# Performance work log

Hardware: AMD Instinct MI355X
Metric: run time of the kernel (lower is better)

## Reference

```python
import jax, jax.numpy as jnp
import numpy as np

B, S, D = 2, 2048, 1024
NH, NKV = 16, 4
HD = D // NH
KVD = NKV * HD
NE, MM = 8, 4
INTER = MM * D // NE  # 512
ROPE_BASE = 10000.0
ALPHA, BETA, GATE, DT = 0.95, 0.3, 0.1, 0.1
MU_MIN, MU_MAX, VMAX = 0.5, 1.5, 3.0


def rms_norm(x):
    # torch F.rms_norm with eps=None -> finfo(dtype).eps, no learned weight
    return x * jax.lax.rsqrt(jnp.mean(x * x, axis=-1, keepdims=True) + jnp.finfo(x.dtype).eps)


def rope_tables(seq_len, dtype):
    inv_freq = 1.0 / ROPE_BASE ** (jnp.arange(0, HD, 2, dtype=jnp.float32) / HD)
    t = jnp.arange(seq_len, dtype=jnp.float32)
    freqs = jnp.outer(t, inv_freq)  # [S, HD/2]
    return jnp.cos(freqs).astype(dtype)[None, None], jnp.sin(freqs).astype(dtype)[None, None]


def apply_rotary(x, cos, sin):
    half = x.shape[-1] // 2
    x1, x2 = x[..., :half], x[..., half:]
    return jnp.concatenate((x1 * cos + x2 * sin, -x1 * sin + x2 * cos), axis=-1)


def attention(n, cq_w, ck_w, cv_w, proj_w, q_gain):
    q = jnp.einsum('bsd,od->bso', n, cq_w).reshape(B, S, NH, HD).transpose(0, 2, 1, 3)
    k = jnp.einsum('bsd,od->bso', n, ck_w).reshape(B, S, NKV, HD).transpose(0, 2, 1, 3)
    v = jnp.einsum('bsd,od->bso', n, cv_w).reshape(B, S, NKV, HD).transpose(0, 2, 1, 3)
    q, k = rms_norm(q), rms_norm(k)
    cos, sin = rope_tables(S, q.dtype)
    q, k = apply_rotary(q, cos, sin), apply_rotary(k, cos, sin)
    q = q * q_gain[None, :, None, None]
    rep = NH // NKV  # GQA: repeat kv heads
    k = jnp.repeat(k, rep, axis=1)
    v = jnp.repeat(v, rep, axis=1)
    scale = 1.0 / np.sqrt(HD).astype(np.float32)
    scores = jnp.einsum('bhqd,bhkd->bhqk', q, k) * scale
    causal = jnp.tril(jnp.ones((S, S), bool))
    scores = jnp.where(causal[None, None], scores, jnp.finfo(scores.dtype).min)
    probs = jax.nn.softmax(scores, axis=-1)
    y = jnp.einsum('bhqk,bhkd->bhqd', probs, v)
    y = y.transpose(0, 2, 1, 3).reshape(B, S, D)
    return jnp.einsum('bsd,od->bso', y, proj_w)


def moe(m, gate_up, down, eids):
    # faithful to TokenRoutedMLP: dense per-expert GEMM, masked accumulate
    flat = m.reshape(-1, D)
    fids = eids.reshape(-1)
    out = jnp.zeros_like(flat)
    for e in range(NE):
        gu = flat @ gate_up[e]                       # [T, 2*INTER]
        g, u = gu[:, :INTER], gu[:, INTER:]
        h = (jax.nn.silu(g) * u) @ down[e]           # [T, D]
        out = out + h * (fids == e)[:, None].astype(flat.dtype)
    return out.reshape(B, S, D)


def setup_inputs():
    key = jax.random.key(0)
    ks = jax.random.split(key, 10)
    w = lambda k, shape: jax.random.normal(k, shape, jnp.float32) * 0.02
    return {
        'x': jax.random.normal(ks[0], (B, S, D), jnp.float32),
        'x0': jax.random.normal(ks[1], (B, S, D), jnp.float32),
        'vel': jnp.zeros((B, S, D), jnp.float32),
        'resid_mix': jnp.stack((jnp.ones(D, jnp.float32), jnp.zeros(D, jnp.float32))),
        'attn_scale': jnp.ones(D, jnp.float32),
        'mlp_scale': jnp.ones(D, jnp.float32),
        'cq_w': w(ks[2], (D, D)),
        'ck_w': w(ks[3], (KVD, D)),
        'cv_w': w(ks[4], (KVD, D)),
        'proj_w': w(ks[5], (D, D)),
        'q_gain': jnp.ones(NH, jnp.float32),
        'mu': jnp.full((D,), 1.0, jnp.float32),
        'gate_up': w(ks[6], (NE, D, 2 * INTER)),
        'down': w(ks[7], (NE, INTER, D)),
        'eids': jax.random.randint(ks[8], (B, S), 0, NE),
    }


def reference(x, x0, vel, resid_mix, attn_scale, mlp_scale, cq_w, ck_w, cv_w, proj_w, q_gain, mu, gate_up, down, eids):
    x = resid_mix[0][None, None, :] * x + resid_mix[1][None, None, :] * x0
    n = rms_norm(x)
    x = x + attn_scale[None, None, :] * attention(n, cq_w, ck_w, cv_w, proj_w, q_gain)
    # PID dynamics
    mu_c = jnp.clip(mu, MU_MIN, MU_MAX)
    v_next = jnp.clip(ALPHA * vel - BETA * (x - mu_c[None, None, :]), -VMAX, VMAX)
    x = x + DT * GATE * v_next
    x = x + mlp_scale[None, None, :] * moe(rms_norm(x), gate_up, down, eids)
    return x, v_next
```

## Files before the change

kernel.cpp:

```cpp
#include <hip/hip_runtime.h>
#include <hip/hip_bf16.h>
#include <math.h>

#define NBATCH 2
#define NSEQ   2048
#define NDIM   1024
#define NHEAD  16
#define NKVH   4
#define HDIM   64
#define KVD    256
#define NEXP   8
#define NINTER 512
#define NTOK   (NBATCH*NSEQ)
#define QKVN   1536
#define MAXTILE 40
#define RMS_EPS 1.1920929e-07f
#define LN_10000 9.210340371976184f
#define QSCALE (0.125f * 1.44269504088896f)
#define DEFER_THR 11.5f

typedef __attribute__((ext_vector_type(8))) short bf16x8;
typedef __attribute__((ext_vector_type(4))) short short4v;
typedef __attribute__((ext_vector_type(4))) float f32x4;

__device__ __forceinline__ short f2b(float f) {
  return __builtin_bit_cast(short, (__bf16)f);
}
__device__ __forceinline__ float b2f(short s) {
  unsigned u = ((unsigned)(unsigned short)s) << 16;
  return __builtin_bit_cast(float, u);
}
__device__ __forceinline__ float ex2(float x) {
  float r; asm("v_exp_f32 %0, %1" : "=v"(r) : "v"(x)); return r;
}
__device__ __forceinline__ void load_lds16(const short* g, short* l) {
  __builtin_amdgcn_global_load_lds((const __attribute__((address_space(1))) void*)g,
                                   (__attribute__((address_space(3))) void*)l, 16, 0, 0);
}

__device__ __forceinline__ float wred64(float v) {
#pragma unroll
  for (int m = 32; m >= 1; m >>= 1) v += __shfl_xor(v, m);
  return v;
}

__global__ __launch_bounds__(256) void k_w_prep(
    const float* __restrict__ cq, const float* __restrict__ ck,
    const float* __restrict__ cv, const float* __restrict__ pw,
    const float* __restrict__ gate_up,
    short* __restrict__ wqkv, short* __restrict__ wproj, short* __restrict__ wgu_t) {
  __shared__ short T[64*66];
  const int bid = blockIdx.x;
  const int t = threadIdx.x;
  if (bid < 2560) {
    const int row = bid;
    const int c = t * 4;
    const float* src; short* dst;
    if (row < 1024)      { src = cq + (size_t)row*NDIM;        dst = wqkv + (size_t)row*NDIM; }
    else if (row < 1280) { src = ck + (size_t)(row-1024)*NDIM; dst = wqkv + (size_t)row*NDIM; }
    else if (row < 1536) { src = cv + (size_t)(row-1280)*NDIM; dst = wqkv + (size_t)row*NDIM; }
    else                 { src = pw + (size_t)(row-1536)*NDIM; dst = wproj + (size_t)(row-1536)*NDIM; }
    float4 v = *(const float4*)(src + c);
    short4v o = {f2b(v.x), f2b(v.y), f2b(v.z), f2b(v.w)};
    *(short4v*)(dst + c) = o;
  } else {
    const int b2 = bid - 2560;
    const int kt = b2 & 15, nt = (b2 >> 4) & 15, e = b2 >> 8;
    const float* ie = gate_up + (size_t)e*1024*1024 + (size_t)(kt*64)*1024 + nt*64;
    short* oe = wgu_t + (size_t)e*1024*1024 + (size_t)(nt*64)*1024 + kt*64;
    const int r = t >> 4, c = (t & 15) * 4;
#pragma unroll
    for (int p = 0; p < 4; ++p) {
      float4 v = *(const float4*)(ie + (size_t)(p*16 + r)*1024 + c);
      T[(p*16 + r)*66 + c + 0] = f2b(v.x);
      T[(p*16 + r)*66 + c + 1] = f2b(v.y);
      T[(p*16 + r)*66 + c + 2] = f2b(v.z);
      T[(p*16 + r)*66 + c + 3] = f2b(v.w);
    }
    __syncthreads();
#pragma unroll
    for (int p = 0; p < 4; ++p) {
      int rr = p*16 + r;
      short4v o = {T[(c+0)*66 + rr], T[(c+1)*66 + rr], T[(c+2)*66 + rr], T[(c+3)*66 + rr]};
      *(short4v*)(oe + (size_t)rr*1024 + c) = o;
    }
  }
}

__global__ __launch_bounds__(256) void k_w_transpose(
    const float* __restrict__ in, short* __restrict__ outp, int KIN, int NIN) {
  __shared__ short T[64*66];
  const int kt = blockIdx.x, nt = blockIdx.y, e = blockIdx.z;
  const float* ie = in + (size_t)e*KIN*NIN + (size_t)(kt*64)*NIN + nt*64;
  short* oe = outp + (size_t)e*NIN*KIN + (size_t)(nt*64)*KIN + kt*64;
  const int t = threadIdx.x;
  const int r = t >> 4, c = (t & 15) * 4;
#pragma unroll
  for (int p = 0; p < 4; ++p) {
    float4 v = *(const float4*)(ie + (size_t)(p*16 + r)*NIN + c);
    T[(p*16 + r)*66 + c + 0] = f2b(v.x);
    T[(p*16 + r)*66 + c + 1] = f2b(v.y);
    T[(p*16 + r)*66 + c + 2] = f2b(v.z);
    T[(p*16 + r)*66 + c + 3] = f2b(v.w);
  }
  __syncthreads();
#pragma unroll
  for (int p = 0; p < 4; ++p) {
    int rr = p*16 + r;
    short4v o = {T[(c+0)*66 + rr], T[(c+1)*66 + rr], T[(c+2)*66 + rr], T[(c+3)*66 + rr]};
    *(short4v*)(oe + (size_t)rr*KIN + c) = o;
  }
}

__global__ __launch_bounds__(256) void k_resid_rms(
    const float* __restrict__ x, const float* __restrict__ x0,
    const float* __restrict__ rmix, short* __restrict__ xr, short* __restrict__ nrm) {
  const int row = blockIdx.x;
  const int t = threadIdx.x;
  const int d = t * 4;
  const size_t base = (size_t)row * NDIM + d;
  float4 a  = *(const float4*)(x  + base);
  float4 b  = *(const float4*)(x0 + base);
  float4 m0 = *(const float4*)(rmix + d);
  float4 m1 = *(const float4*)(rmix + NDIM + d);
  float4 r;
  r.x = m0.x*a.x + m1.x*b.x;
  r.y = m0.y*a.y + m1.y*b.y;
  r.z = m0.z*a.z + m1.z*b.z;
  r.w = m0.w*a.w + m1.w*b.w;
  float ss = r.x*r.x + r.y*r.y + r.z*r.z + r.w*r.w;
  ss = wred64(ss);
  __shared__ float wsum[4];
  if ((t & 63) == 0) wsum[t >> 6] = ss;
  __syncthreads();
  float tot = wsum[0] + wsum[1] + wsum[2] + wsum[3];
  float rms = rsqrtf(tot * (1.0f/NDIM) + RMS_EPS);
  short4v xo = {f2b(r.x), f2b(r.y), f2b(r.z), f2b(r.w)};
  short4v no = {f2b(r.x*rms), f2b(r.y*rms), f2b(r.z*rms), f2b(r.w*rms)};
  *(short4v*)(xr + base) = xo;
  *(short4v*)(nrm + base) = no;
}

template <int MODE>
__global__ __launch_bounds__(256) void k_gemm_mfma(
    const short* __restrict__ A, int lda,
    const short* __restrict__ Bw, int K, int N,
    short* __restrict__ Cb, float* __restrict__ Cf, int ldc,
    const int* __restrict__ rowmap, const int* __restrict__ tiletab,
    const int* __restrict__ meta, const float* __restrict__ mscale) {
  __shared__ short sA[128*32];
  __shared__ short sB[128*32];
  int row0, end = 0x7fffffff, e = 0;
  if (MODE == 0) {
    row0 = blockIdx.y * 128;
  } else {
    e = tiletab[2*blockIdx.y];
    if (e < 0) return;
    row0 = tiletab[2*blockIdx.y + 1];
    end = meta[1 + e];
  }
  const int t = threadIdx.x;
  const int w = t >> 6, l = t & 63;
  const int wr = (w >> 1) * 64, wc = (w & 1) * 64;
  const int lrow = l & 15, lk8 = (l >> 4) * 8;
  const int srow0 = w*16 + (l >> 2);
  const int scol = (l & 3) * 8;
  const short* Bp = Bw + (size_t)e * N * K + (size_t)(blockIdx.x * 128) * K;
  const short* gA0;
  const short* gA1;
  if (MODE == 1) {
    int s0 = row0 + srow0;      if (s0 >= NTOK) s0 = NTOK - 1;
    int s1 = row0 + 64 + srow0; if (s1 >= NTOK) s1 = NTOK - 1;
    gA0 = A + (size_t)rowmap[s0] * lda + scol;
    gA1 = A + (size_t)rowmap[s1] * lda + scol;
  } else {
    gA0 = A + (size_t)(row0 + srow0) * lda + scol;
    gA1 = A + (size_t)(row0 + 64 + srow0) * lda + scol;
  }
  const short* gB0 = Bp + (size_t)srow0 * K + scol;
  const short* gB1 = Bp + (size_t)(64 + srow0) * K + scol;
  short* lA0 = sA + (w*16)*32;
  short* lA1 = sA + (64 + w*16)*32;
  short* lB0 = sB + (w*16)*32;
  short* lB1 = sB + (64 + w*16)*32;
  f32x4 acc[4][4];
#pragma unroll
  for (int m = 0; m < 4; ++m)
#pragma unroll
    for (int n = 0; n < 4; ++n) acc[m][n] = 0.f;
  for (int k0 = 0; k0 < K; k0 += 32) {
    __syncthreads();
    load_lds16(gA0, lA0);
    load_lds16(gA1, lA1);
    load_lds16(gB0, lB0);
    load_lds16(gB1, lB1);
    gA0 += 32; gA1 += 32; gB0 += 32; gB1 += 32;
    __syncthreads();
    bf16x8 af[4], bfr[4];
#pragma unroll
    for (int m = 0; m < 4; ++m)
      af[m] = *(const bf16x8*)&sA[(wr + m*16 + lrow)*32 + lk8];
#pragma unroll
    for (int n = 0; n < 4; ++n)
      bfr[n] = *(const bf16x8*)&sB[(wc + n*16 + lrow)*32 + lk8];
#pragma unroll
    for (int m = 0; m < 4; ++m)
#pragma unroll
      for (int n = 0; n < 4; ++n)
        acc[m][n] = __builtin_amdgcn_mfma_f32_16x16x32_bf16(af[m], bfr[n], acc[m][n], 0, 0, 0);
  }
  const int col0 = blockIdx.x * 128;
  if (MODE <= 1) {
#pragma unroll
    for (int m = 0; m < 4; ++m) {
#pragma unroll
      for (int r = 0; r < 4; ++r) {
        int rr = row0 + wr + m*16 + (l >> 4)*4 + r;
        if (rr < end) {
#pragma unroll
          for (int n = 0; n < 4; ++n)
            Cb[(size_t)rr * ldc + col0 + wc + n*16 + lrow] = f2b(acc[m][n][r]);
        }
      }
    }
  } else {
#pragma unroll
    for (int m = 0; m < 4; ++m) {
#pragma unroll
      for (int r = 0; r < 4; ++r) {
        int slot = row0 + wr + m*16 + (l >> 4)*4 + r;
        if (slot < end) {
          int tok = rowmap[slot];
#pragma unroll
          for (int n = 0; n < 4; ++n) {
            int cc = col0 + wc + n*16 + lrow;
            Cf[(size_t)tok * ldc + cc] += mscale[cc] * acc[m][n][r];
          }
        }
      }
    }
  }
}

__global__ __launch_bounds__(256) void k_qk_norm_rope(
    short* __restrict__ qkv, const float* __restrict__ q_gain) {
  const int row = blockIdx.x;
  const int t = threadIdx.x;
  const int w = t >> 6, lane = t & 63;
  const int s = row & (NSEQ - 1);
  const int fi = lane & 31;
  const float fr = (float)s * expf(-(float)fi * (LN_10000 / 32.0f));
  const float co = cosf(fr), si = sinf(fr);
#pragma unroll
  for (int h = w; h < NHEAD; h += 4) {
    short* p = qkv + (size_t)row*QKVN + h*HDIM + lane;
    float v = b2f(*p);
    float ssum = wred64(v*v);
    float rr = rsqrtf(ssum * (1.0f/HDIM) + RMS_EPS);
    float vn = v * rr;
    float partner = __shfl_xor(vn, 32);
    float o = (lane < 32) ? (vn*co + partner*si) : (vn*co - partner*si);
    *p = f2b(o * q_gain[h] * QSCALE);
  }
  if (w < NKVH) {
    short* p = qkv + (size_t)row*QKVN + 1024 + w*HDIM + lane;
    float v = b2f(*p);
    float ssum = wred64(v*v);
    float rr = rsqrtf(ssum * (1.0f/HDIM) + RMS_EPS);
    float vn = v * rr;
    float partner = __shfl_xor(vn, 32);
    float o = (lane < 32) ? (vn*co + partner*si) : (vn*co - partner*si);
    *p = f2b(o);
  }
}

__global__ __launch_bounds__(256) void k_transpose_v(
    const short* __restrict__ qkv, short* __restrict__ vbT) {
  __shared__ short T[64*72];
  const int blk = blockIdx.x;
  const int st = blk & 31, kh = (blk >> 5) & 3, b = blk >> 7;
  const int t = threadIdx.x;
#pragma unroll
  for (int i = 0; i < 2; ++i) {
    int c = t + i*256;
    int s = c >> 3, d0 = (c & 7) * 8;
    bf16x8 v = *(const bf16x8*)(qkv + (size_t)(b*NSEQ + st*64 + s)*QKVN + 1280 + kh*HDIM + d0);
#pragma unroll
    for (int j = 0; j < 8; ++j) T[(d0 + j)*72 + s] = v[j];
  }
  __syncthreads();
#pragma unroll
  for (int i = 0; i < 2; ++i) {
    int c = t + i*256;
    int d = c >> 3, s0 = (c & 7) * 8;
    *(bf16x8*)(vbT + (size_t)((b*NKVH + kh)*HDIM + d)*NSEQ + st*64 + s0) = *(bf16x8*)&T[d*72 + s0];
  }
}

__global__ __launch_bounds__(256) void k_attn_mfma(
    const short* __restrict__ qkv, const short* __restrict__ vbT, short* __restrict__ y) {
  __shared__ short Ks[2][64*72];
  __shared__ short Vt[2][64*72];
  __shared__ short Ps[64*72];
  const int t = threadIdx.x;
  const int l = t & 63, w = t >> 6;
  const int lrow = l & 15, g = l >> 4, lk8 = g * 8;
  const int bid = blockIdx.x;
  int qt = bid & 15;
  const int h = (bid >> 4) & 15, b = bid >> 8;
  if (b & 1) qt = 15 - qt;
  const int kh = h >> 2;
  bf16x8 qf[2][2];
#pragma unroll
  for (int qra = 0; qra < 2; ++qra) {
    int qrow_g = b*NSEQ + qt*128 + qra*64 + w*16 + lrow;
#pragma unroll
    for (int hf = 0; hf < 2; ++hf)
      qf[qra][hf] = *(const bf16x8*)(qkv + (size_t)qrow_g*QKVN + h*HDIM + hf*32 + lk8);
  }
  const int r0a = t >> 3;
  const int d0a = (t & 7) * 8;
  const short* kgbase = qkv + 1024 + (size_t)kh*HDIM;
  const short* vgbase = vbT + (size_t)((b*NKVH + kh)*HDIM)*NSEQ;
  bf16x8 kr0, kr1, vr0, vr1;
#define LOADKV(KT) do { \
    kr0 = *(const bf16x8*)(kgbase + (size_t)(b*NSEQ + (KT)*64 + r0a)*QKVN + d0a); \
    kr1 = *(const bf16x8*)(kgbase + (size_t)(b*NSEQ + (KT)*64 + r0a + 32)*QKVN + d0a); \
    vr0 = *(const bf16x8*)(vgbase + (size_t)r0a*NSEQ + (KT)*64 + d0a); \
    vr1 = *(const bf16x8*)(vgbase + (size_t)(r0a + 32)*NSEQ + (KT)*64 + d0a); \
  } while (0)
  float m_i[2] = {-INFINITY, -INFINITY};
  float l_i[2] = {0.f, 0.f};
  f32x4 O[2][4];
#pragma unroll
  for (int qra = 0; qra < 2; ++qra)
#pragma unroll
    for (int db = 0; db < 4; ++db) O[qra][db] = 0.f;
  const int ktmax = 2*qt + 1;
  LOADKV(0);
  for (int kt = 0; kt <= ktmax; ++kt) {
    const int buf = kt & 1;
    *(bf16x8*)&Ks[buf][r0a*72 + d0a] = kr0;
    *(bf16x8*)&Ks[buf][(r0a + 32)*72 + d0a] = kr1;
    *(bf16x8*)&Vt[buf][r0a*72 + d0a] = vr0;
    *(bf16x8*)&Vt[buf][(r0a + 32)*72 + d0a] = vr1;
    __syncthreads();
    if (kt < ktmax) LOADKV(kt + 1);
    bf16x8 kf[4][2];
#pragma unroll
    for (int nb = 0; nb < 4; ++nb) {
      kf[nb][0] = *(const bf16x8*)&Ks[buf][(nb*16 + lrow)*72 + lk8];
      kf[nb][1] = *(const bf16x8*)&Ks[buf][(nb*16 + lrow)*72 + 32 + lk8];
    }
    const int qra0 = (kt == ktmax) ? 1 : 0;
    bf16x8 pf[2][2];
#pragma unroll
    for (int qra = 0; qra < 2; ++qra) {
      if (qra >= qra0) {
        f32x4 sc[4];
#pragma unroll
        for (int nb = 0; nb < 4; ++nb) sc[nb] = 0.f;
        __builtin_amdgcn_s_setprio(1);
#pragma unroll
        for (int nb = 0; nb < 4; ++nb) {
          sc[nb] = __builtin_amdgcn_mfma_f32_16x16x32_bf16(kf[nb][0], qf[qra][0], sc[nb], 0, 0, 0);
          sc[nb] = __builtin_amdgcn_mfma_f32_16x16x32_bf16(kf[nb][1], qf[qra][1], sc[nb], 0, 0, 0);
        }
        __builtin_amdgcn_s_setprio(0);
        if (kt >= 2*qt) {
          int qg = qt*128 + qra*64 + w*16 + lrow;
#pragma unroll
          for (int nb = 0; nb < 4; ++nb)
#pragma unroll
            for (int r = 0; r < 4; ++r)
              if (kt*64 + nb*16 + g*4 + r > qg) sc[nb][r] = -INFINITY;
        }
        float rm = sc[0][0];
#pragma unroll
        for (int nb = 0; nb < 4; ++nb)
#pragma unroll
          for (int r = 0; r < 4; ++r) rm = fmaxf(rm, sc[nb][r]);
        rm = fmaxf(rm, __shfl_xor(rm, 16));
        rm = fmaxf(rm, __shfl_xor(rm, 32));
        if (!__all(rm <= m_i[qra] + DEFER_THR)) {
          float mn = fmaxf(m_i[qra], rm);
          float fac = ex2(m_i[qra] - mn);
          l_i[qra] *= fac;
          m_i[qra] = mn;
#pragma unroll
          for (int r = 0; r < 4; ++r) {
            float ff = __shfl(fac, g*4 + r);
#pragma unroll
            for (int db = 0; db < 4; ++db) O[qra][db][r] *= ff;
          }
        }
        float rs = 0.f;
#pragma unroll
        for (int nb = 0; nb < 4; ++nb) {
#pragma unroll
          for (int r = 0; r < 4; ++r) {
            float p = ex2(sc[nb][r] - m_i[qra]);
            sc[nb][r] = p;
            rs += p;
          }
        }
        rs += __shfl_xor(rs, 16);
        rs += __shfl_xor(rs, 32);
        l_i[qra] += rs;
        short* prow = &Ps[(w*16 + lrow)*72];
#pragma unroll
        for (int nb = 0; nb < 4; ++nb) {
          short4v pk = {f2b(sc[nb][0]), f2b(sc[nb][1]), f2b(sc[nb][2]), f2b(sc[nb][3])};
          *(short4v*)(prow + nb*16 + g*4) = pk;
        }
        pf[qra][0] = *(const bf16x8*)&Ps[(w*16 + lrow)*72 + lk8];
        pf[qra][1] = *(const bf16x8*)&Ps[(w*16 + lrow)*72 + 32 + lk8];
      }
    }
    __builtin_amdgcn_s_setprio(1);
#pragma unroll
    for (int db = 0; db < 4; ++db) {
      bf16x8 vf0 = *(const bf16x8*)&Vt[buf][(db*16 + lrow)*72 + lk8];
      bf16x8 vf1 = *(const bf16x8*)&Vt[buf][(db*16 + lrow)*72 + 32 + lk8];
      if (qra0 == 0) {
        O[0][db] = __builtin_amdgcn_mfma_f32_16x16x32_bf16(pf[0][0], vf0, O[0][db], 0, 0, 0);
        O[0][db] = __builtin_amdgcn_mfma_f32_16x16x32_bf16(pf[0][1], vf1, O[0][db], 0, 0, 0);
      }
      O[1][db] = __builtin_amdgcn_mfma_f32_16x16x32_bf16(pf[1][0], vf0, O[1][db], 0, 0, 0);
      O[1][db] = __builtin_amdgcn_mfma_f32_16x16x32_bf16(pf[1][1], vf1, O[1][db], 0, 0, 0);
    }
    __builtin_amdgcn_s_setprio(0);
  }
#undef LOADKV
#pragma unroll
  for (int qra = 0; qra < 2; ++qra) {
    float linv = 1.0f / l_i[qra];
#pragma unroll
    for (int r = 0; r < 4; ++r) {
      float inv = __shfl(linv, g*4 + r);
      int rowo = b*NSEQ + qt*128 + qra*64 + w*16 + g*4 + r;
#pragma unroll
      for (int db = 0; db < 4; ++db)
        y[(size_t)rowo*NDIM + h*HDIM + db*16 + lrow] = f2b(O[qra][db][r] * inv);
    }
  }
}

__global__ __launch_bounds__(256) void k_fuse_vel(
    const short* __restrict__ xr, const short* __restrict__ aout,
    const float* __restrict__ vel, const float* __restrict__ ascale,
    const float* __restrict__ mu, float* __restrict__ out, short* __restrict__ mbuf) {
  const int row = blockIdx.x;
  const int t = threadIdx.x;
  const int d = t * 4;
  const size_t base = (size_t)row * NDIM + d;
  short4v a4 = *(const short4v*)(xr + base);
  short4v o4 = *(const short4v*)(aout + base);
  float4 vv = *(const float4*)(vel + base);
  float4 as = *(const float4*)(ascale + d);
  float4 mu4 = *(const float4*)(mu + d);
  float xs[4], vns[4];
  const float asl[4] = {as.x, as.y, as.z, as.w};
  const float mul[4] = {mu4.x, mu4.y, mu4.z, mu4.w};
  const float vvl[4] = {vv.x, vv.y, vv.z, vv.w};
#pragma unroll
  for (int i = 0; i < 4; ++i) {
    float x1 = b2f(a4[i]) + asl[i] * b2f(o4[i]);
    float muc = fminf(fmaxf(mul[i], 0.5f), 1.5f);
    float vn = fminf(fmaxf(0.95f*vvl[i] - 0.3f*(x1 - muc), -3.f), 3.f);
    xs[i] = x1 + 0.01f*vn;
    vns[i] = vn;
  }
  float4 x2 = {xs[0], xs[1], xs[2], xs[3]};
  float4 vnq = {vns[0], vns[1], vns[2], vns[3]};
  *(float4*)(out + base) = x2;
  *(float4*)(out + (size_t)NTOK*NDIM + base) = vnq;
  float ss = xs[0]*xs[0] + xs[1]*xs[1] + xs[2]*xs[2] + xs[3]*xs[3];
  ss = wred64(ss);
  __shared__ float wsum[4];
  if ((t & 63) == 0) wsum[t >> 6] = ss;
  __syncthreads();
  float tot = wsum[0] + wsum[1] + wsum[2] + wsum[3];
  float rms = rsqrtf(tot * (1.0f/NDIM) + RMS_EPS);
  short4v m4 = {f2b(xs[0]*rms), f2b(xs[1]*rms), f2b(xs[2]*rms), f2b(xs[3]*rms)};
  *(short4v*)(mbuf + base) = m4;
}

__global__ __launch_bounds__(256) void k_route(
    const int* __restrict__ eids, int* __restrict__ rowmap,
    int* __restrict__ tiletab, int* __restrict__ meta) {
  __shared__ int cnt[NEXP];
  __shared__ int ctr[NEXP];
  const int t = threadIdx.x;
  if (t < NEXP) cnt[t] = 0;
  __syncthreads();
  for (int i = t; i < NTOK; i += 256) atomicAdd(&cnt[eids[i]], 1);
  __syncthreads();
  if (t == 0) {
    int off = 0, tile = 0;
    for (int e = 0; e < NEXP; ++e) {
      ctr[e] = off;
      int nt_e = (cnt[e] + 127) >> 7;
      for (int j = 0; j < nt_e; ++j) { tiletab[2*tile] = e; tiletab[2*tile+1] = off + j*128; ++tile; }
      off += cnt[e];
      meta[1 + e] = off;
    }
    meta[0] = tile;
    for (int j = tile; j < MAXTILE; ++j) { tiletab[2*j] = -1; tiletab[2*j+1] = 0; }
  }
  __syncthreads();
  for (int i = t; i < NTOK; i += 256) {
    int e = eids[i];
    int slot = atomicAdd(&ctr[e], 1);
    rowmap[slot] = i;
  }
}

__global__ __launch_bounds__(256) void k_silu(
    const short* __restrict__ gu, short* __restrict__ hb) {
  int gid = blockIdx.x * 256 + threadIdx.x;
  int row = gid >> 7, c4 = (gid & 127) * 4;
  short4v g = *(const short4v*)(gu + (size_t)row*1024 + c4);
  short4v u = *(const short4v*)(gu + (size_t)row*1024 + 512 + c4);
  short4v o;
#pragma unroll
  for (int i = 0; i < 4; ++i) {
    float gf = b2f(g[i]), uf = b2f(u[i]);
    o[i] = f2b(gf / (1.0f + __expf(-gf)) * uf);
  }
  *(short4v*)(hb + (size_t)row*512 + c4) = o;
}

extern "C" void kernel_launch(void* const* d_in, const int* in_sizes, int n_in,
                              void* d_out, int out_size, void* d_ws, size_t ws_size,
                              hipStream_t stream) {
  const float* x      = (const float*)d_in[0];
  const float* x0     = (const float*)d_in[1];
  const float* vel    = (const float*)d_in[2];
  const float* rmix   = (const float*)d_in[3];
  const float* ascale = (const float*)d_in[4];
  const float* mscale = (const float*)d_in[5];
  const float* cq_w   = (const float*)d_in[6];
  const float* ck_w   = (const float*)d_in[7];
  const float* cv_w   = (const float*)d_in[8];
  const float* proj_w = (const float*)d_in[9];
  const float* q_gain = (const float*)d_in[10];
  const float* mu     = (const float*)d_in[11];
  const float* gate_up= (const float*)d_in[12];
  const float* down   = (const float*)d_in[13];
  const int*   eids   = (const int*)d_in[14];
  float* out = (float*)d_out;
  char* base = (char*)d_ws;

  const size_t MB = 1024*1024;
  short* wqkv  = (short*)base;
  short* wproj = (short*)(base + 3*MB);
  int*   rowmap  = (int*)(base + 5*MB);
  int*   tiletab = rowmap + NTOK;
  int*   meta    = tiletab + 2*MAXTILE;
  short* wgu_t = (short*)(base + 6*MB);
  short* hbuf  = wgu_t;
  short* xr    = (short*)(base + 22*MB);
  short* gu    = xr;
  short* nbuf  = (short*)(base + 30*MB);
  short* ybuf  = nbuf;
  short* mbuf  = nbuf;
  short* wdn_t = nbuf;
  short* qkv   = (short*)(base + 38*MB);
  short* aout  = qkv;
  short* vbT   = (short*)(base + 50*MB);

  k_w_prep<<<4608, 256, 0, stream>>>(cq_w, ck_w, cv_w, proj_w, gate_up, wqkv, wproj, wgu_t);
  k_resid_rms<<<NTOK, 256, 0, stream>>>(x, x0, rmix, xr, nbuf);
  k_gemm_mfma<0><<<dim3(QKVN/128, NTOK/128), 256, 0, stream>>>(
      nbuf, NDIM, wqkv, NDIM, QKVN, qkv, nullptr, QKVN, nullptr, nullptr, nullptr, nullptr);
  k_qk_norm_rope<<<NTOK, 256, 0, stream>>>(qkv, q_gain);
  k_transpose_v<<<NBATCH*NKVH*(NSEQ/64), 256, 0, stream>>>(qkv, vbT);
  k_attn_mfma<<<NBATCH*NHEAD*(NSEQ/128), 256, 0, stream>>>(qkv, vbT, ybuf);
  k_gemm_mfma<0><<<dim3(NDIM/128, NTOK/128), 256, 0, stream>>>(
      ybuf, NDIM, wproj, NDIM, NDIM, aout, nullptr, NDIM, nullptr, nullptr, nullptr, nullptr);
  k_fuse_vel<<<NTOK, 256, 0, stream>>>(xr, aout, vel, ascale, mu, out, mbuf);
  k_route<<<1, 256, 0, stream>>>(eids, rowmap, tiletab, meta);
  k_gemm_mfma<1><<<dim3(1024/128, MAXTILE), 256, 0, stream>>>(
      mbuf, NDIM, wgu_t, NDIM, 1024, gu, nullptr, 1024, rowmap, tiletab, meta, nullptr);
  k_w_transpose<<<dim3(8, 16, 8), 256, 0, stream>>>(down, wdn_t, 512, 1024);
  k_silu<<<(NTOK*512)/(4*256), 256, 0, stream>>>(gu, hbuf);
  k_gemm_mfma<2><<<dim3(NDIM/128, MAXTILE), 256, 0, stream>>>(
      hbuf, NINTER, wdn_t, NINTER, NDIM, nullptr, out, NDIM, rowmap, tiletab, meta, mscale);
}
```

Baseline: 231.4 us.

## Double-buffer LDS tiles in MFMA GEMM and raise wave priority around MFMAs

Gives the GEMM kernel two LDS buffers per operand and prefetches the next K-slice into the spare buffer while MFMAs run on the current one. This removes one of the two barriers per K iteration and lets global-to-LDS traffic overlap with compute. It also wraps the MFMA block in s_setprio to favour waves that are issuing matrix ops. The cost is double the LDS per block (32 KB instead of 16 KB), which may lower occupancy.

Measured after the change: 227.0 us. No clear change (-1.9%).

```diff
diff --git a/kernel.cpp b/kernel.cpp
--- a/kernel.cpp
+++ b/kernel.cpp
@@ -148,8 +148,8 @@
     short* __restrict__ Cb, float* __restrict__ Cf, int ldc,
     const int* __restrict__ rowmap, const int* __restrict__ tiletab,
     const int* __restrict__ meta, const float* __restrict__ mscale) {
-  __shared__ short sA[128*32];
-  __shared__ short sB[128*32];
+  __shared__ short sA[2][128*32];
+  __shared__ short sB[2][128*32];
   int row0, end = 0x7fffffff, e = 0;
   if (MODE == 0) {
     row0 = blockIdx.y * 128;
@@ -179,35 +179,43 @@
   }
   const short* gB0 = Bp + (size_t)srow0 * K + scol;
   const short* gB1 = Bp + (size_t)(64 + srow0) * K + scol;
-  short* lA0 = sA + (w*16)*32;
-  short* lA1 = sA + (64 + w*16)*32;
-  short* lB0 = sB + (w*16)*32;
-  short* lB1 = sB + (64 + w*16)*32;
+  const int lo0 = (w*16)*32;
+  const int lo1 = (64 + w*16)*32;
   f32x4 acc[4][4];
 #pragma unroll
   for (int m = 0; m < 4; ++m)
 #pragma unroll
     for (int n = 0; n < 4; ++n) acc[m][n] = 0.f;
+  load_lds16(gA0, sA[0] + lo0);
+  load_lds16(gA1, sA[0] + lo1);
+  load_lds16(gB0, sB[0] + lo0);
+  load_lds16(gB1, sB[0] + lo1);
+  gA0 += 32; gA1 += 32; gB0 += 32; gB1 += 32;
+  int cur = 0;
   for (int k0 = 0; k0 < K; k0 += 32) {
     __syncthreads();
-    load_lds16(gA0, lA0);
-    load_lds16(gA1, lA1);
-    load_lds16(gB0, lB0);
-    load_lds16(gB1, lB1);
-    gA0 += 32; gA1 += 32; gB0 += 32; gB1 += 32;
-    __syncthreads();
+    if (k0 + 32 < K) {
+      load_lds16(gA0, sA[cur^1] + lo0);
+      load_lds16(gA1, sA[cur^1] + lo1);
+      load_lds16(gB0, sB[cur^1] + lo0);
+      load_lds16(gB1, sB[cur^1] + lo1);
+      gA0 += 32; gA1 += 32; gB0 += 32; gB1 += 32;
+    }
     bf16x8 af[4], bfr[4];
 #pragma unroll
     for (int m = 0; m < 4; ++m)
-      af[m] = *(const bf16x8*)&sA[(wr + m*16 + lrow)*32 + lk8];
+      af[m] = *(const bf16x8*)&sA[cur][(wr + m*16 + lrow)*32 + lk8];
 #pragma unroll
     for (int n = 0; n < 4; ++n)
-      bfr[n] = *(const bf16x8*)&sB[(wc + n*16 + lrow)*32 + lk8];
+      bfr[n] = *(const bf16x8*)&sB[cur][(wc + n*16 + lrow)*32 + lk8];
+    __builtin_amdgcn_s_setprio(1);
 #pragma unroll
     for (int m = 0; m < 4; ++m)
 #pragma unroll
       for (int n = 0; n < 4; ++n)
         acc[m][n] = __builtin_amdgcn_mfma_f32_16x16x32_bf16(af[m], bfr[n], acc[m][n], 0, 0, 0);
+    __builtin_amdgcn_s_setprio(0);
+    cur ^= 1;
   }
   const int col0 = blockIdx.x * 128;
   if (MODE <= 1) {
```
